# Kernel optimization log

Measured on AMD Instinct MI355X. Metric: run time of the kernel, lower is better.

## Reference

```python
import jax, jax.numpy as jnp
import numpy as np

EPS = 1e-5
K = 3

def _bn(x, g, b):
    # training-mode BatchNorm2d: batch stats over (N,H,W), biased variance
    m = jnp.mean(x, axis=(0, 2, 3), keepdims=True)
    v = jnp.var(x, axis=(0, 2, 3), keepdims=True)
    return (x - m) * jax.lax.rsqrt(v + EPS) * g[None, :, None, None] + b[None, :, None, None]

def _gelu(x):
    return jax.nn.gelu(x, approximate=False)

def _dyn_dw(x, aw1, ab1, aw2, ab2):
    # dynamic depthwise conv: per-sample k^2 softmax weights shared over channels
    b, c, h, w = x.shape
    gap = jnp.mean(x, axis=(2, 3))                              # (b,c)
    h1 = jax.nn.relu(jnp.einsum('oc,bc->bo', aw1, gap) + ab1)   # (b,c//8)
    kw = jax.nn.softmax(jnp.einsum('oc,bc->bo', aw2, h1) + ab2, axis=1)  # (b,k^2)
    xp = jnp.pad(x, ((0, 0), (0, 0), (1, 1), (1, 1)))
    out = jnp.zeros_like(x)
    idx = 0
    for i in range(K):
        for j in range(K):
            out = out + kw[:, idx, None, None, None] * xp[:, :, i:i + h, j:j + w]
            idx += 1
    return out

def _channel_att(x, w1, w2):
    avg = jnp.mean(x, axis=(2, 3))        # (b,C)
    mx = jnp.max(x, axis=(2, 3))          # (b,C)
    def fc(v):
        return jnp.einsum('oc,bc->bo', w2, jax.nn.relu(jnp.einsum('oc,bc->bo', w1, v)))
    s = jax.nn.sigmoid(fc(avg) + fc(mx))  # (b,C)
    return s[:, :, None, None] * x

def _forward(x, w1, b1, g1, be1, aw1, ab1, aw2, ab2, g2, be2,
             ca_w1, ca_w2, pw, pb, g3, be3, sw, sb):
    b, n, d = x.shape
    h = w = int(np.sqrt(n))
    residual = x
    xi = jnp.transpose(x.reshape(b, h, w, d), (0, 3, 1, 2))       # (b,d,h,w)
    # pw_expand: 1x1 conv -> GELU -> BN
    y = jnp.einsum('oc,bchw->bohw', w1, xi) + b1[None, :, None, None]
    y = _bn(_gelu(y), g1, be1)                                    # (b,4d,h,w)
    # dw_conv: dynamic depthwise -> GELU -> BN -> channel attention
    y = _dyn_dw(y, aw1, ab1, aw2, ab2)
    y = _bn(_gelu(y), g2, be2)
    y = _channel_att(y, ca_w1, ca_w2)
    # spatial attention
    avg_o = jnp.mean(y, axis=1, keepdims=True)
    max_o = jnp.max(y, axis=1, keepdims=True)
    sp_in = jnp.concatenate([avg_o, max_o], axis=1)               # (b,2,h,w)
    sp = jax.lax.conv_general_dilated(sp_in, sw, (1, 1), ((3, 3), (3, 3)),
                                      dimension_numbers=('NCHW', 'OIHW', 'NCHW'))
    sp = jax.nn.sigmoid(sp + sb[None, :, None, None])
    y = y * sp
    # pw_project: 1x1 conv -> BN
    y = jnp.einsum('oc,bchw->bohw', pw, y) + pb[None, :, None, None]
    y = _bn(y, g3, be3)
    y = jnp.transpose(y, (0, 2, 3, 1)).reshape(b, n, d)
    return residual + y

def setup_inputs() -> dict:
    key = jax.random.key(0)
    ks = jax.random.split(key, 16)
    d, C = 256, 1024
    def rn(k, shape, fan):
        return jax.random.normal(k, shape, jnp.float32) * np.float32(np.sqrt(2.0 / fan))
    return {
        'x': jax.random.normal(ks[0], (8, 1024, d), jnp.float32),
        'w1': rn(ks[1], (C, d), d), 'b1': jnp.zeros((C,), jnp.float32),
        'g1': jnp.ones((C,), jnp.float32), 'be1': jnp.zeros((C,), jnp.float32),
        'aw1': rn(ks[2], (C // 8, C), C), 'ab1': jnp.zeros((C // 8,), jnp.float32),
        'aw2': rn(ks[3], (K * K, C // 8), C // 8), 'ab2': jnp.zeros((K * K,), jnp.float32),
        'g2': jnp.ones((C,), jnp.float32), 'be2': jnp.zeros((C,), jnp.float32),
        'ca_w1': rn(ks[4], (C // 16, C), C), 'ca_w2': rn(ks[5], (C, C // 16), C // 16),
        'pw': rn(ks[6], (d, C), C), 'pb': jnp.zeros((d,), jnp.float32),
        'g3': jnp.ones((d,), jnp.float32), 'be3': jnp.zeros((d,), jnp.float32),
        'sw': rn(ks[7], (1, 2, 7, 7), 2 * 49), 'sb': jnp.zeros((1,), jnp.float32),
    }

def reference(x, w1, b1, g1, be1, aw1, ab1, aw2, ab2, g2, be2,
              ca_w1, ca_w2, pw, pb, g3, be3, sw, sb):
    return _forward(x, w1, b1, g1, be1, aw1, ab1, aw2, ab2, g2, be2,
                    ca_w1, ca_w2, pw, pb, g3, be3, sw, sb)
```

## Files before the change

### kernel.cpp

```cpp
#include <hip/hip_runtime.h>
#include <math.h>

constexpr int B = 8;
constexpr int D = 256;
constexpr int C = 1024;
constexpr int H = 32, W = 32;
constexpr int P = H * W;
constexpr int M = B * P;
constexpr float EPS = 1e-5f;

typedef unsigned short u16;
typedef unsigned int u32;
typedef __attribute__((ext_vector_type(8))) short short8;
typedef __attribute__((ext_vector_type(4))) float floatx4;

constexpr size_t WS_CHSUM1 = 0;
constexpr size_t WS_CHSQ1  = 1024;
constexpr size_t WS_GAPSUM = 2048;
constexpr size_t WS_CHSUM3 = 10240;
constexpr size_t WS_CHSQ3  = 10496;
constexpr size_t WS_CHSUM2 = 10752;
constexpr size_t WS_CHSQ2  = 11776;
constexpr size_t WS_BSUM2  = 12800;
constexpr size_t WS_UMAX2  = 20992;
constexpr size_t WS_UMAXN2 = 29184;
constexpr size_t WS_ACC_COUNT = 37376;
constexpr size_t WS_SCALE1 = 37376;
constexpr size_t WS_SHIFT1 = 38400;
constexpr size_t WS_KW     = 39424;
constexpr size_t WS_SCALE2 = 39680;
constexpr size_t WS_SHIFT2 = 40704;
constexpr size_t WS_SATT   = 41728;
constexpr size_t WS_AVGO   = 49920;
constexpr size_t WS_MAXO   = 58112;
constexpr size_t WS_SP     = 66304;
constexpr size_t WS_PRE    = 74496;
constexpr size_t WS_T1B    = 2171648;
constexpr size_t WS_T2B    = 6365952;
constexpr size_t WS_XB     = 10560256;
constexpr size_t WS_W1B    = 11608832;
constexpr size_t WS_PWB    = 11739904;
constexpr size_t WS_PWBF   = 11870976;
constexpr size_t WS_BIAS2  = 12919552;

__device__ __forceinline__ float gelu_exact(float v) {
    return 0.5f * v * (1.0f + erff(v * 0.70710678118654752440f));
}

__device__ __forceinline__ u16 f2bf(float f) {
    u32 u = __float_as_uint(f);
    u += 0x7fff + ((u >> 16) & 1);
    return (u16)(u >> 16);
}

__device__ __forceinline__ float bf2f(u16 v) {
    return __uint_as_float(((u32)v) << 16);
}

__device__ __forceinline__ u32 fkey(float f) {
    u32 u = __float_as_uint(f);
    return (u & 0x80000000u) ? ~u : (u | 0x80000000u);
}
__device__ __forceinline__ float fkeyinv(u32 k) {
    return __uint_as_float((k & 0x80000000u) ? (k ^ 0x80000000u) : ~k);
}

#define GLOAD(SRC, DST) __builtin_amdgcn_global_load_lds( \
    (const __attribute__((address_space(1))) void*)(SRC), \
    (__attribute__((address_space(3))) void*)(DST), 16, 0, 0)

__global__ __launch_bounds__(256) void cvt_all_kernel(const float* __restrict__ x,
                                                      const float* __restrict__ w1,
                                                      u16* __restrict__ xb,
                                                      u16* __restrict__ w1b,
                                                      float* __restrict__ acc_zero) {
    const int i = blockIdx.x * 256 + threadIdx.x;
    if (i < (int)WS_ACC_COUNT) acc_zero[i] = 0.f;
    const float* src;
    u16* dst;
    int off;
    if (i < 524288) { src = x;  dst = xb;  off = i; }
    else            { src = w1; dst = w1b; off = i - 524288; }
    const float4 v = *(const float4*)(src + (size_t)off * 4);
    uint2 o;
    o.x = ((u32)f2bf(v.x)) | ((u32)f2bf(v.y) << 16);
    o.y = ((u32)f2bf(v.z)) | ((u32)f2bf(v.w) << 16);
    *(uint2*)(dst + (size_t)off * 4) = o;
}

template<int KD, int EPI, int NS, int MB, int NB>
__global__ __launch_bounds__(256) void mfma_gemm_kernel(
    const u16* __restrict__ A,
    const u16* __restrict__ Bw,
    const float* __restrict__ bias,
    const float* __restrict__ bias_post,
    const float* __restrict__ avg_o,
    const float* __restrict__ max_o,
    const float* __restrict__ swp,
    const float* __restrict__ sbp,
    void* __restrict__ outv,
    float* __restrict__ csum,
    float* __restrict__ csq,
    float* __restrict__ gsum)
{
    constexpr int MI = MB / 32;
    constexpr int NJ = NB / 32;
    constexpr int ABUF = MB * 32;
    constexpr int BBUF = NB * 32;
    constexpr int BUFSZ = ABUF + BBUF;
    constexpr int GA = MB / 64;
    constexpr int GB = NB / 64;
    constexpr int LD = GA + GB;
    static_assert(LD == 3, "vmcnt literals assume 3 loads per chunk");
    constexpr int NCH = KD / 32;
    constexpr int GX = NS / NB;
    constexpr int NWG = (M / MB) * GX;
    constexpr int CPX = NWG / 8;
    extern __shared__ u16 smem[];
    const int t = threadIdx.x;
    const int lane = t & 63;

    const int lin = blockIdx.y * GX + blockIdx.x;
    const int swz = (lin & 7) * CPX + (lin >> 3);
    const int bx = swz % GX;
    const int by = swz / GX;
    const int row0 = by * MB;
    const int col0 = bx * NB;
    const int bb = row0 >> 10;

    const int wv = t >> 6;
    const int wrow = (wv >> 1) * (MB / 2);
    const int wcol = (wv & 1) * (NB / 2);
    const int lm = lane & 15;
    const int lk8 = (lane >> 4) * 8;
    const int srow = t >> 2;
    const int scol = (t & 3) * 8;
    const u16* gA = A + (size_t)(row0 + srow) * KD + scol;
    const u16* gB = Bw + (EPI == 1 ? (size_t)bb * NS * KD : (size_t)0)
                       + (size_t)(col0 + srow) * KD + scol;
    const float* biasp = bias + (EPI == 1 ? bb * NS : 0);

    const floatx4 zero = {0.f, 0.f, 0.f, 0.f};
    floatx4 acc[MI][NJ];
#pragma unroll
    for (int i = 0; i < MI; ++i)
#pragma unroll
        for (int j = 0; j < NJ; ++j) acc[i][j] = zero;

    auto stage = [&](u16* buf, int c) {
        const int kk = c * 32;
        u16* As = buf;
        u16* Bs = buf + ABUF;
#pragma unroll
        for (int g = 0; g < GA; ++g)
            GLOAD(gA + (size_t)g * 64 * KD + kk, As + g * 2048 + t * 8);
#pragma unroll
        for (int g = 0; g < GB; ++g)
            GLOAD(gB + (size_t)g * 64 * KD + kk, Bs + g * 2048 + t * 8);
    };
    auto compute = [&](const u16* buf) {
        const u16* As = buf;
        const u16* Bs = buf + ABUF;
        short8 af[MI], bf[NJ];
#pragma unroll
        for (int i = 0; i < MI; ++i)
            af[i] = *(const short8*)(As + (wrow + i * 16 + lm) * 32 + lk8);
#pragma unroll
        for (int j = 0; j < NJ; ++j)
            bf[j] = *(const short8*)(Bs + (wcol + j * 16 + lm) * 32 + lk8);
#pragma unroll
        for (int i = 0; i < MI; ++i)
#pragma unroll
            for (int j = 0; j < NJ; ++j)
                acc[i][j] = __builtin_amdgcn_mfma_f32_16x16x32_bf16(af[i], bf[j], acc[i][j], 0, 0, 0);
    };

    stage(smem, 0);
    if (NCH > 1) stage(smem + BUFSZ, 1);

    float* ext = (float*)smem + 9216;
    if constexpr (EPI == 1) {
        const int p0 = (by & 7) * MB;
        const int h0 = p0 >> 5;
        const int bbase = bb * P;
        for (int e = t; e < 640; e += 256) {
            const bool isM = e >= 320;
            const int idx = isM ? e - 320 : e;
            const int r = idx >> 5, w = idx & 31;
            const int hh = h0 - 3 + r;
            float v = 0.f;
            if (hh >= 0 && hh < H) v = (isM ? max_o : avg_o)[bbase + hh * W + w];
            ext[e] = v;
        }
        if (t < 98) ext[640 + t] = swp[t];
        __syncthreads();
        if (t < 128) {
            const int hl = t >> 5, w = t & 31;
            float a = sbp[0];
#pragma unroll
            for (int i = 0; i < 7; ++i) {
                const int r = hl + i;
#pragma unroll
                for (int j = 0; j < 7; ++j) {
                    const int ww = w + j - 3;
                    if (ww < 0 || ww >= W) continue;
                    a = fmaf(ext[640 + i * 7 + j], ext[r * 32 + ww], a);
                    a = fmaf(ext[640 + 49 + i * 7 + j], ext[320 + r * 32 + ww], a);
                }
            }
            ext[768 + t] = 1.0f / (1.0f + expf(-a));
        }
    }

    int cur = 0;
    for (int c = 0; c < NCH; ++c) {
        if (c + 2 < NCH) {
            const int nb3 = (cur + 2 >= 3) ? cur - 1 : cur + 2;
            stage(smem + nb3 * BUFSZ, c + 2);
            asm volatile("s_waitcnt vmcnt(6)" ::: "memory");
        } else if (c + 1 < NCH) {
            asm volatile("s_waitcnt vmcnt(3)" ::: "memory");
        } else {
            asm volatile("s_waitcnt vmcnt(0)" ::: "memory");
        }
        __builtin_amdgcn_s_barrier();
        compute(smem + cur * BUFSZ);
        asm volatile("s_waitcnt lgkmcnt(0)" ::: "memory");
        __builtin_amdgcn_s_barrier();
        cur = (cur + 1 >= 3) ? 0 : cur + 1;
    }

    float colsum[NJ], colsq[NJ];
#pragma unroll
    for (int j = 0; j < NJ; ++j) { colsum[j] = 0.f; colsq[j] = 0.f; }

    if (EPI == 0) {
        u16* Cs = smem;
#pragma unroll
        for (int i = 0; i < MI; ++i) {
#pragma unroll
            for (int r = 0; r < 4; ++r) {
                const int lrow = wrow + i * 16 + (lane >> 4) * 4 + r;
#pragma unroll
                for (int j = 0; j < NJ; ++j) {
                    const int lcol = wcol + j * 16 + lm;
                    const float tv = gelu_exact(acc[i][j][r] + biasp[col0 + lcol]);
                    Cs[lrow * NB + lcol] = f2bf(tv);
                    colsum[j] += tv;
                    colsq[j] = fmaf(tv, tv, colsq[j]);
                }
            }
        }
        __syncthreads();
        constexpr int TPR = NB / 8;
        constexpr int RPP = 256 / TPR;
        u16* outp = (u16*)outv;
#pragma unroll
        for (int pp = 0; pp < MB / RPP; ++pp) {
            const int r = pp * RPP + t / TPR;
            const int cc = (t % TPR) * 8;
            *(uint4*)(outp + (size_t)(row0 + r) * NS + col0 + cc) =
                *(const uint4*)(Cs + r * NB + cc);
        }
    } else {
        float* Cs = (float*)smem;
#pragma unroll
        for (int i = 0; i < MI; ++i) {
#pragma unroll
            for (int r = 0; r < 4; ++r) {
                const int lrow = wrow + i * 16 + (lane >> 4) * 4 + r;
                const float rs = ext[768 + lrow];
#pragma unroll
                for (int j = 0; j < NJ; ++j) {
                    const int lcol = wcol + j * 16 + lm;
                    const float tv = rs * (acc[i][j][r] + biasp[col0 + lcol])
                                   + bias_post[col0 + lcol];
                    Cs[lrow * NB + lcol] = tv;
                    colsum[j] += tv;
                    colsq[j] = fmaf(tv, tv, colsq[j]);
                }
            }
        }
        __syncthreads();
        constexpr int TPR = NB / 4;
        constexpr int RPP = 256 / TPR;
        float* outp = (float*)outv;
#pragma unroll
        for (int pp = 0; pp < MB / RPP; ++pp) {
            const int r = pp * RPP + t / TPR;
            const int cc = (t % TPR) * 4;
            *(float4*)(outp + (size_t)(row0 + r) * NS + col0 + cc) =
                *(const float4*)(Cs + r * NB + cc);
        }
    }

#pragma unroll
    for (int j = 0; j < NJ; ++j) {
        float s = colsum[j];
        float q = colsq[j];
        s += __shfl_xor(s, 16); s += __shfl_xor(s, 32);
        q += __shfl_xor(q, 16); q += __shfl_xor(q, 32);
        if (lane < 16) {
            const int c = col0 + wcol + j * 16 + lm;
            atomicAdd(&csum[c], s);
            atomicAdd(&csq[c], q);
            if (EPI == 0) atomicAdd(&gsum[bb * NS + c], s);
        }
    }
}

__global__ __launch_bounds__(1024) void dynmlp_kernel(const float* __restrict__ chsum1,
                                                      const float* __restrict__ chsq1,
                                                      const float* __restrict__ gapsum,
                                                      const float* __restrict__ g1,
                                                      const float* __restrict__ be1,
                                                      const float* __restrict__ aw1,
                                                      const float* __restrict__ ab1,
                                                      const float* __restrict__ aw2,
                                                      const float* __restrict__ ab2,
                                                      float* __restrict__ scale1,
                                                      float* __restrict__ shift1,
                                                      float* __restrict__ kw) {
    const int b = blockIdx.x;
    const int t = threadIdx.x;
    const int wave = t >> 6, lane = t & 63;
    __shared__ float g[1024];
    __shared__ float h1[128];
    __shared__ float logits[12];
    {
        const float m = chsum1[t] * (1.0f / (float)M);
        const float var = chsq1[t] * (1.0f / (float)M) - m * m;
        const float rstd = rsqrtf(var + EPS);
        const float sc = rstd * g1[t];
        const float sh = be1[t] - m * sc;
        if (b == 0) { scale1[t] = sc; shift1[t] = sh; }
        g[t] = gapsum[b * C + t] * (1.0f / (float)P) * sc + sh;
    }
    __syncthreads();
#pragma unroll
    for (int k = 0; k < 8; ++k) {
        const int u = wave * 8 + k;
        const float4* wr = (const float4*)(aw1 + (size_t)u * C);
        float s = 0.f;
#pragma unroll
        for (int ch = 0; ch < 4; ++ch) {
            const float4 wv = wr[lane + 64 * ch];
            const float4 sv = *(const float4*)(g + 4 * lane + 256 * ch);
            s += wv.x * sv.x + wv.y * sv.y + wv.z * sv.z + wv.w * sv.w;
        }
#pragma unroll
        for (int off = 1; off < 64; off <<= 1) s += __shfl_xor(s, off);
        if (lane == 0) h1[u] = fmaxf(s + ab1[u], 0.f);
    }
    __syncthreads();
    if (wave < 9) {
        float s = aw2[wave * 128 + lane] * h1[lane]
                + aw2[wave * 128 + 64 + lane] * h1[64 + lane];
#pragma unroll
        for (int off = 1; off < 64; off <<= 1) s += __shfl_xor(s, off);
        if (lane == 0) logits[wave] = s + ab2[wave];
    }
    __syncthreads();
    if (t == 0) {
        float mx = logits[0];
        for (int i = 1; i < 9; ++i) mx = fmaxf(mx, logits[i]);
        float e[9], den = 0.f;
        for (int i = 0; i < 9; ++i) { e[i] = expf(logits[i] - mx); den += e[i]; }
        const float inv = 1.0f / den;
        for (int i = 0; i < 9; ++i) kw[b * 9 + i] = e[i] * inv;
    }
}

__global__ __launch_bounds__(256) void dwconv_kernel(const u16* __restrict__ t1b,
                                                     const float* __restrict__ scale1,
                                                     const float* __restrict__ shift1,
                                                     const float* __restrict__ kw,
                                                     u16* __restrict__ t2b,
                                                     float* __restrict__ chsum2,
                                                     float* __restrict__ chsq2,
                                                     float* __restrict__ bsum2,
                                                     u32* __restrict__ umax2,
                                                     u32* __restrict__ umaxn2) {
    __shared__ u16 rows[3 * 32 * 256];
    const int lin = blockIdx.y * 4 + blockIdx.x;
    const int xcd = lin & 7;
    const int i7 = lin >> 3;
    const int b = i7 >> 4;
    const int r4 = i7 & 15;
    const int h = xcd * 4 + (r4 >> 2);
    const int cq = r4 & 3;
    const int t = threadIdx.x;

    const u16* gbase = t1b + (size_t)b * P * C + cq * 256;
#pragma unroll
    for (int i = 0; i < 12; ++i) {
        const int lin2 = i * 256 + t;
        const int chunk = lin2 >> 5;
        const int r = chunk >> 5;
        const int w = chunk & 31;
        const int off8 = (lin2 & 31) * 8;
        const int hr = h + r - 1;
        uint4 v = {0u, 0u, 0u, 0u};
        if (hr >= 0 && hr < H)
            v = *(const uint4*)(gbase + (size_t)(hr * W + w) * C + off8);
        *(uint4*)(&rows[chunk * 256 + off8]) = v;
    }
    __syncthreads();

    const int c = t;
    const int gc = cq * 256 + c;
    float kk[9];
#pragma unroll
    for (int i = 0; i < 9; ++i) kk[i] = kw[b * 9 + i];
    const float sc = scale1[gc];
    const float sh = shift1[gc];
    float scm[3], shm[3];
    scm[0] = (h > 0)     ? sc : 0.f;  shm[0] = (h > 0)     ? sh : 0.f;
    scm[1] = sc;                      shm[1] = sh;
    scm[2] = (h < H - 1) ? sc : 0.f;  shm[2] = (h < H - 1) ? sh : 0.f;

    const u16* rp0 = rows + c;
#define DWVAL(ri, w) fmaf(bf2f(rp0[((ri) * 32 + (w)) * 256]), scm[ri], shm[ri])

    float vm0 = 0.f, vm1 = 0.f, vm2 = 0.f;
    float vc0 = DWVAL(0, 0), vc1 = DWVAL(1, 0), vc2 = DWVAL(2, 0);
    float vp0 = DWVAL(0, 1), vp1 = DWVAL(1, 1), vp2 = DWVAL(2, 1);

    float s = 0.f, q = 0.f, mx = -INFINITY, mn = INFINITY;
    u16* orow = t2b + ((size_t)b * P + h * W) * C + gc;
    for (int w = 0; w < W; ++w) {
        float acc;
        acc = kk[0] * vm0;
        acc = fmaf(kk[1], vc0, acc);
        acc = fmaf(kk[2], vp0, acc);
        acc = fmaf(kk[3], vm1, acc);
        acc = fmaf(kk[4], vc1, acc);
        acc = fmaf(kk[5], vp1, acc);
        acc = fmaf(kk[6], vm2, acc);
        acc = fmaf(kk[7], vc2, acc);
        acc = fmaf(kk[8], vp2, acc);
        const float y = gelu_exact(acc);
        orow[(size_t)w * C] = f2bf(y);
        s += y;
        q = fmaf(y, y, q);
        mx = fmaxf(mx, y);
        mn = fminf(mn, y);
        vm0 = vc0; vc0 = vp0;
        vm1 = vc1; vc1 = vp1;
        vm2 = vc2; vc2 = vp2;
        if (w + 2 < W) {
            vp0 = DWVAL(0, w + 2);
            vp1 = DWVAL(1, w + 2);
            vp2 = DWVAL(2, w + 2);
        } else {
            vp0 = 0.f; vp1 = 0.f; vp2 = 0.f;
        }
    }
#undef DWVAL
    atomicAdd(&chsum2[gc], s);
    atomicAdd(&chsq2[gc], q);
    atomicAdd(&bsum2[b * C + gc], s);
    atomicMax(&umax2[b * C + gc], fkey(mx));
    atomicMax(&umaxn2[b * C + gc], fkey(-mn));
}

__global__ __launch_bounds__(1024) void chatt_kernel(const float* __restrict__ chsum2,
                                                     const float* __restrict__ chsq2,
                                                     const float* __restrict__ bsum2,
                                                     const u32* __restrict__ umax2,
                                                     const u32* __restrict__ umaxn2,
                                                     const float* __restrict__ g2,
                                                     const float* __restrict__ be2,
                                                     const float* __restrict__ caw1,
                                                     const float* __restrict__ caw2,
                                                     float* __restrict__ scale2,
                                                     float* __restrict__ shift2,
                                                     float* __restrict__ s_att) {
    const int b = blockIdx.x;
    const int t = threadIdx.x;
    const int wave = t >> 6, lane = t & 63;
    __shared__ float la[1024], lx[1024], ha[64], hm[64];
    {
        const float m = chsum2[t] * (1.0f / (float)M);
        const float var = chsq2[t] * (1.0f / (float)M) - m * m;
        const float rstd = rsqrtf(var + EPS);
        const float sc = rstd * g2[t];
        const float sh = be2[t] - m * sc;
        if (b == 0) { scale2[t] = sc; shift2[t] = sh; }
        la[t] = bsum2[b * C + t] * (1.0f / (float)P) * sc + sh;
        const float mx = fkeyinv(umax2[b * C + t]);
        const float mn = -fkeyinv(umaxn2[b * C + t]);
        lx[t] = (sc >= 0.f ? mx : mn) * sc + sh;
    }
    __syncthreads();
#pragma unroll
    for (int k = 0; k < 8; ++k) {
        const int u = wave * 8 + k;
        const int row = u & 63;
        const float* src = (u < 64) ? la : lx;
        const float4* wr = (const float4*)(caw1 + (size_t)row * C);
        float s = 0.f;
#pragma unroll
        for (int ch = 0; ch < 4; ++ch) {
            const float4 wv = wr[lane + 64 * ch];
            const float4 sv = *(const float4*)(src + 4 * lane + 256 * ch);
            s += wv.x * sv.x + wv.y * sv.y + wv.z * sv.z + wv.w * sv.w;
        }
#pragma unroll
        for (int off = 1; off < 64; off <<= 1) s += __shfl_xor(s, off);
        if (lane == 0) {
            s = fmaxf(s, 0.f);
            if (u < 64) ha[row] = s; else hm[row] = s;
        }
    }
    __syncthreads();
    {
        const float4* w2 = (const float4*)(caw2 + (size_t)t * 64);
        float s = 0.f;
#pragma unroll
        for (int j = 0; j < 16; ++j) {
            const float4 wv = w2[j];
            s += wv.x * (ha[j * 4 + 0] + hm[j * 4 + 0]);
            s += wv.y * (ha[j * 4 + 1] + hm[j * 4 + 1]);
            s += wv.z * (ha[j * 4 + 2] + hm[j * 4 + 2]);
            s += wv.w * (ha[j * 4 + 3] + hm[j * 4 + 3]);
        }
        s_att[b * C + t] = 1.0f / (1.0f + expf(-s));
    }
}

__global__ __launch_bounds__(256) void yqfold_kernel(const u16* __restrict__ t2b,
                                                     const float* __restrict__ scale2,
                                                     const float* __restrict__ shift2,
                                                     const float* __restrict__ s_att,
                                                     const float* __restrict__ pw,
                                                     float* __restrict__ avg_o,
                                                     float* __restrict__ max_o,
                                                     u16* __restrict__ pwb,
                                                     float* __restrict__ bias2) {
    const int bid = blockIdx.x;
    const int t = threadIdx.x;
    const int wave = t >> 6, lane = t & 63;
    __shared__ float r0[4], r1[4];
    if (bid < M) {
        const int row = bid;
        const int b = row >> 10;
        const int c0 = t * 4;
        const uint2 vv = *(const uint2*)(t2b + (size_t)row * C + c0);
        const float v0 = bf2f((u16)(vv.x & 0xffff));
        const float v1 = bf2f((u16)(vv.x >> 16));
        const float v2 = bf2f((u16)(vv.y & 0xffff));
        const float v3 = bf2f((u16)(vv.y >> 16));
        const float4 sc = *(const float4*)(scale2 + c0);
        const float4 sh = *(const float4*)(shift2 + c0);
        const float4 sa = *(const float4*)(s_att + (size_t)b * C + c0);
        const float y0 = fmaf(v0, sc.x, sh.x) * sa.x;
        const float y1 = fmaf(v1, sc.y, sh.y) * sa.y;
        const float y2 = fmaf(v2, sc.z, sh.z) * sa.z;
        const float y3 = fmaf(v3, sc.w, sh.w) * sa.w;
        float s = (y0 + y1) + (y2 + y3);
        float mx = fmaxf(fmaxf(y0, y1), fmaxf(y2, y3));
#pragma unroll
        for (int off = 32; off > 0; off >>= 1) {
            s += __shfl_down(s, off);
            mx = fmaxf(mx, __shfl_down(mx, off));
        }
        if (lane == 0) { r0[wave] = s; r1[wave] = mx; }
        __syncthreads();
        if (t == 0) {
            const float S = r0[0] + r0[1] + r0[2] + r0[3];
            const float Mx = fmaxf(fmaxf(r1[0], r1[1]), fmaxf(r1[2], r1[3]));
            avg_o[row] = S * (1.0f / (float)C);
            max_o[row] = Mx;
        }
    } else {
        const int bd = bid - M;
        const int b = bd >> 8;
        const int d = bd & 255;
        const int c0 = t * 4;
        const float4 wv = *(const float4*)(pw + (size_t)d * C + c0);
        const float4 sc = *(const float4*)(scale2 + c0);
        const float4 sh = *(const float4*)(shift2 + c0);
        const float4 sa = *(const float4*)(s_att + (size_t)b * C + c0);
        uint2 o;
        o.x = ((u32)f2bf(wv.x * sc.x * sa.x)) | ((u32)f2bf(wv.y * sc.y * sa.y) << 16);
        o.y = ((u32)f2bf(wv.z * sc.z * sa.z)) | ((u32)f2bf(wv.w * sc.w * sa.w) << 16);
        *(uint2*)(pwb + ((size_t)b * D + d) * C + c0) = o;
        float s = wv.x * sh.x * sa.x + wv.y * sh.y * sa.y
                + wv.z * sh.z * sa.z + wv.w * sh.w * sa.w;
#pragma unroll
        for (int off = 1; off < 64; off <<= 1) s += __shfl_xor(s, off);
        if (lane == 0) r0[wave] = s;
        __syncthreads();
        if (t == 0) bias2[bd] = r0[0] + r0[1] + r0[2] + r0[3];
    }
}

__global__ __launch_bounds__(256) void final_kernel(const float* __restrict__ x,
                                                    const float* __restrict__ pre,
                                                    const float* __restrict__ chsum3,
                                                    const float* __restrict__ chsq3,
                                                    const float* __restrict__ g3,
                                                    const float* __restrict__ be3,
                                                    float* __restrict__ out) {
    __shared__ float lsc[256], lsh[256];
    const int t = threadIdx.x;
    {
        const float m = chsum3[t] * (1.0f / (float)M);
        const float var = chsq3[t] * (1.0f / (float)M) - m * m;
        const float rstd = rsqrtf(var + EPS);
        const float sc = rstd * g3[t];
        lsc[t] = sc;
        lsh[t] = be3[t] - m * sc;
    }
    __syncthreads();
    const int i = blockIdx.x * 256 + t;
    const int e = i * 4;
    const int d = e & 255;
    const float4 xv = *(const float4*)(x + e);
    const float4 pv = *(const float4*)(pre + e);
    const float4 sc = *(const float4*)(lsc + d);
    const float4 sh = *(const float4*)(lsh + d);
    float4 o;
    o.x = xv.x + fmaf(pv.x, sc.x, sh.x);
    o.y = xv.y + fmaf(pv.y, sc.y, sh.y);
    o.z = xv.z + fmaf(pv.z, sc.z, sh.z);
    o.w = xv.w + fmaf(pv.w, sc.w, sh.w);
    *(float4*)(out + e) = o;
}

extern "C" void kernel_launch(void* const* d_in, const int* in_sizes, int n_in,
                              void* d_out, int out_size, void* d_ws, size_t ws_size,
                              hipStream_t stream) {
    const float* x    = (const float*)d_in[0];
    const float* w1   = (const float*)d_in[1];
    const float* b1   = (const float*)d_in[2];
    const float* g1   = (const float*)d_in[3];
    const float* be1  = (const float*)d_in[4];
    const float* aw1  = (const float*)d_in[5];
    const float* ab1  = (const float*)d_in[6];
    const float* aw2  = (const float*)d_in[7];
    const float* ab2  = (const float*)d_in[8];
    const float* g2   = (const float*)d_in[9];
    const float* be2  = (const float*)d_in[10];
    const float* caw1 = (const float*)d_in[11];
    const float* caw2 = (const float*)d_in[12];
    const float* pw   = (const float*)d_in[13];
    const float* pb   = (const float*)d_in[14];
    const float* g3   = (const float*)d_in[15];
    const float* be3  = (const float*)d_in[16];
    const float* sw   = (const float*)d_in[17];
    const float* sb   = (const float*)d_in[18];
    float* out = (float*)d_out;
    float* ws = (float*)d_ws;

    float* chsum1  = ws + WS_CHSUM1;
    float* chsq1   = ws + WS_CHSQ1;
    float* gapsum  = ws + WS_GAPSUM;
    float* chsum3  = ws + WS_CHSUM3;
    float* chsq3   = ws + WS_CHSQ3;
    float* chsum2  = ws + WS_CHSUM2;
    float* chsq2   = ws + WS_CHSQ2;
    float* bsum2   = ws + WS_BSUM2;
    u32*   umax2   = (u32*)(ws + WS_UMAX2);
    u32*   umaxn2  = (u32*)(ws + WS_UMAXN2);
    float* scale1  = ws + WS_SCALE1;
    float* shift1  = ws + WS_SHIFT1;
    float* kw      = ws + WS_KW;
    float* scale2  = ws + WS_SCALE2;
    float* shift2  = ws + WS_SHIFT2;
    float* s_att   = ws + WS_SATT;
    float* avg_o   = ws + WS_AVGO;
    float* max_o   = ws + WS_MAXO;
    float* pre     = ws + WS_PRE;
    float* bias2   = ws + WS_BIAS2;
    u16* t1b  = (u16*)(ws + WS_T1B);
    u16* t2b  = (u16*)(ws + WS_T2B);
    u16* xb   = (u16*)(ws + WS_XB);
    u16* w1b  = (u16*)(ws + WS_W1B);
    u16* pwbf = (u16*)(ws + WS_PWBF);

    cvt_all_kernel<<<dim3(2304), 256, 0, stream>>>(x, w1, xb, w1b, ws);
    mfma_gemm_kernel<256, 0, C, 128, 64><<<dim3(C / 64, M / 128), 256, 36864, stream>>>(
        xb, w1b, b1, nullptr, nullptr, nullptr, nullptr, nullptr,
        t1b, chsum1, chsq1, gapsum);
    dynmlp_kernel<<<dim3(B), 1024, 0, stream>>>(chsum1, chsq1, gapsum, g1, be1,
                                                aw1, ab1, aw2, ab2, scale1, shift1, kw);
    dwconv_kernel<<<dim3(4, B * H), 256, 0, stream>>>(t1b, scale1, shift1, kw, t2b,
                                                      chsum2, chsq2, bsum2, umax2, umaxn2);
    chatt_kernel<<<dim3(B), 1024, 0, stream>>>(chsum2, chsq2, bsum2, umax2, umaxn2,
                                               g2, be2, caw1, caw2, scale2, shift2, s_att);
    yqfold_kernel<<<dim3(M + B * D), 256, 0, stream>>>(t2b, scale2, shift2, s_att, pw,
                                                       avg_o, max_o, pwbf, bias2);
    mfma_gemm_kernel<1024, 1, D, 128, 64><<<dim3(D / 64, M / 128), 256, 40448, stream>>>(
        t2b, pwbf, bias2, pb, avg_o, max_o, sw, sb,
        pre, chsum3, chsq3, nullptr);
    final_kernel<<<dim3((M * D / 4) / 256), 256, 0, stream>>>(x, pre, chsum3, chsq3, g3, be3, out);
}
```

Measured before the change: 198.9 us.

## Split K across two wave groups in the second GEMM with LDS reduction

Adds a WSPLIT template parameter so the projection GEMM (K=1024, only 256 workgroups) runs with 512 threads. Two independent 4-wave groups each pipeline half of the K chunks in their own LDS buffers, then partial accumulators are summed through shared memory before the epilogue. This aims to raise occupancy and latency hiding for a GEMM with few tiles. In exchange it uses roughly double the LDS per block and adds an extra reduction pass with barriers.

```diff
diff --git a/kernel.cpp b/kernel.cpp
--- a/kernel.cpp
+++ b/kernel.cpp
@@ -88,8 +88,8 @@
     *(uint2*)(dst + (size_t)off * 4) = o;
 }
 
-template<int KD, int EPI, int NS, int MB, int NB>
-__global__ __launch_bounds__(256) void mfma_gemm_kernel(
+template<int KD, int EPI, int NS, int MB, int NB, int WSPLIT>
+__global__ __launch_bounds__(256 * WSPLIT) void mfma_gemm_kernel(
     const u16* __restrict__ A,
     const u16* __restrict__ Bw,
     const float* __restrict__ bias,
@@ -103,6 +103,7 @@
     float* __restrict__ csq,
     float* __restrict__ gsum)
 {
+    constexpr int NT = 256 * WSPLIT;
     constexpr int MI = MB / 32;
     constexpr int NJ = NB / 32;
     constexpr int ABUF = MB * 32;
@@ -113,12 +114,17 @@
     constexpr int LD = GA + GB;
     static_assert(LD == 3, "vmcnt literals assume 3 loads per chunk");
     constexpr int NCH = KD / 32;
+    constexpr int NCHG = NCH / WSPLIT;
     constexpr int GX = NS / NB;
     constexpr int NWG = (M / MB) * GX;
     constexpr int CPX = NWG / 8;
     extern __shared__ u16 smem[];
     const int t = threadIdx.x;
     const int lane = t & 63;
+    const int wv = t >> 6;
+    const int grp = (WSPLIT == 2) ? (wv >> 2) : 0;
+    const int wg = wv & 3;
+    const int tg = t & 255;
 
     const int lin = blockIdx.y * GX + blockIdx.x;
     const int swz = (lin & 7) * CPX + (lin >> 3);
@@ -128,18 +134,20 @@
     const int col0 = bx * NB;
     const int bb = row0 >> 10;
 
-    const int wv = t >> 6;
-    const int wrow = (wv >> 1) * (MB / 2);
-    const int wcol = (wv & 1) * (NB / 2);
+    const int wrow = (wg >> 1) * (MB / 2);
+    const int wcol = (wg & 1) * (NB / 2);
     const int lm = lane & 15;
     const int lk8 = (lane >> 4) * 8;
-    const int srow = t >> 2;
-    const int scol = (t & 3) * 8;
+    const int srow = tg >> 2;
+    const int scol = (tg & 3) * 8;
     const u16* gA = A + (size_t)(row0 + srow) * KD + scol;
     const u16* gB = Bw + (EPI == 1 ? (size_t)bb * NS * KD : (size_t)0)
                        + (size_t)(col0 + srow) * KD + scol;
     const float* biasp = bias + (EPI == 1 ? bb * NS : 0);
 
+    u16* gsmem = smem + grp * (3 * BUFSZ);
+    const int kbase = grp * NCHG;
+
     const floatx4 zero = {0.f, 0.f, 0.f, 0.f};
     floatx4 acc[MI][NJ];
 #pragma unroll
@@ -148,15 +156,15 @@
         for (int j = 0; j < NJ; ++j) acc[i][j] = zero;
 
     auto stage = [&](u16* buf, int c) {
-        const int kk = c * 32;
+        const int kk = (kbase + c) * 32;
         u16* As = buf;
         u16* Bs = buf + ABUF;
 #pragma unroll
         for (int g = 0; g < GA; ++g)
-            GLOAD(gA + (size_t)g * 64 * KD + kk, As + g * 2048 + t * 8);
+            GLOAD(gA + (size_t)g * 64 * KD + kk, As + g * 2048 + tg * 8);
 #pragma unroll
         for (int g = 0; g < GB; ++g)
-            GLOAD(gB + (size_t)g * 64 * KD + kk, Bs + g * 2048 + t * 8);
+            GLOAD(gB + (size_t)g * 64 * KD + kk, Bs + g * 2048 + tg * 8);
     };
     auto compute = [&](const u16* buf) {
         const u16* As = buf;
@@ -175,15 +183,15 @@
                 acc[i][j] = __builtin_amdgcn_mfma_f32_16x16x32_bf16(af[i], bf[j], acc[i][j], 0, 0, 0);
     };
 
-    stage(smem, 0);
-    if (NCH > 1) stage(smem + BUFSZ, 1);
-
-    float* ext = (float*)smem + 9216;
+    stage(gsmem, 0);
+    if (NCHG > 1) stage(gsmem + BUFSZ, 1);
+
+    float* ext = (float*)(smem + (size_t)WSPLIT * 3 * BUFSZ);
     if constexpr (EPI == 1) {
         const int p0 = (by & 7) * MB;
         const int h0 = p0 >> 5;
         const int bbase = bb * P;
-        for (int e = t; e < 640; e += 256) {
+        for (int e = t; e < 640; e += NT) {
             const bool isM = e >= 320;
             const int idx = isM ? e - 320 : e;
             const int r = idx >> 5, w = idx & 31;
@@ -213,21 +221,49 @@
     }
 
     int cur = 0;
-    for (int c = 0; c < NCH; ++c) {
-        if (c + 2 < NCH) {
+    for (int c = 0; c < NCHG; ++c) {
+        if (c + 2 < NCHG) {
             const int nb3 = (cur + 2 >= 3) ? cur - 1 : cur + 2;
-            stage(smem + nb3 * BUFSZ, c + 2);
+            stage(gsmem + nb3 * BUFSZ, c + 2);
             asm volatile("s_waitcnt vmcnt(6)" ::: "memory");
-        } else if (c + 1 < NCH) {
+        } else if (c + 1 < NCHG) {
             asm volatile("s_waitcnt vmcnt(3)" ::: "memory");
         } else {
             asm volatile("s_waitcnt vmcnt(0)" ::: "memory");
         }
         __builtin_amdgcn_s_barrier();
-        compute(smem + cur * BUFSZ);
+        compute(gsmem + cur * BUFSZ);
         asm volatile("s_waitcnt lgkmcnt(0)" ::: "memory");
         __builtin_amdgcn_s_barrier();
         cur = (cur + 1 >= 3) ? 0 : cur + 1;
+    }
+
+    if constexpr (WSPLIT == 2) {
+        float* red = (float*)(smem + 3 * BUFSZ);
+        if (grp == 1) {
+#pragma unroll
+            for (int i = 0; i < MI; ++i)
+#pragma unroll
+                for (int r = 0; r < 4; ++r) {
+                    const int lrow = wrow + i * 16 + (lane >> 4) * 4 + r;
+#pragma unroll
+                    for (int j = 0; j < NJ; ++j)
+                        red[lrow * NB + wcol + j * 16 + lm] = acc[i][j][r];
+                }
+        }
+        __syncthreads();
+        if (grp == 0) {
+#pragma unroll
+            for (int i = 0; i < MI; ++i)
+#pragma unroll
+                for (int r = 0; r < 4; ++r) {
+                    const int lrow = wrow + i * 16 + (lane >> 4) * 4 + r;
+#pragma unroll
+                    for (int j = 0; j < NJ; ++j)
+                        acc[i][j][r] += red[lrow * NB + wcol + j * 16 + lm];
+                }
+        }
+        __syncthreads();
     }
 
     float colsum[NJ], colsq[NJ];
@@ -253,7 +289,7 @@
         }
         __syncthreads();
         constexpr int TPR = NB / 8;
-        constexpr int RPP = 256 / TPR;
+        constexpr int RPP = NT / TPR;
         u16* outp = (u16*)outv;
 #pragma unroll
         for (int pp = 0; pp < MB / RPP; ++pp) {
@@ -264,26 +300,28 @@
         }
     } else {
         float* Cs = (float*)smem;
-#pragma unroll
-        for (int i = 0; i < MI; ++i) {
-#pragma unroll
-            for (int r = 0; r < 4; ++r) {
-                const int lrow = wrow + i * 16 + (lane >> 4) * 4 + r;
-                const float rs = ext[768 + lrow];
-#pragma unroll
-                for (int j = 0; j < NJ; ++j) {
-                    const int lcol = wcol + j * 16 + lm;
-                    const float tv = rs * (acc[i][j][r] + biasp[col0 + lcol])
-                                   + bias_post[col0 + lcol];
-                    Cs[lrow * NB + lcol] = tv;
-                    colsum[j] += tv;
-                    colsq[j] = fmaf(tv, tv, colsq[j]);
+        if (grp == 0) {
+#pragma unroll
+            for (int i = 0; i < MI; ++i) {
+#pragma unroll
+                for (int r = 0; r < 4; ++r) {
+                    const int lrow = wrow + i * 16 + (lane >> 4) * 4 + r;
+                    const float rs = ext[768 + lrow];
+#pragma unroll
+                    for (int j = 0; j < NJ; ++j) {
+                        const int lcol = wcol + j * 16 + lm;
+                        const float tv = rs * (acc[i][j][r] + biasp[col0 + lcol])
+                                       + bias_post[col0 + lcol];
+                        Cs[lrow * NB + lcol] = tv;
+                        colsum[j] += tv;
+                        colsq[j] = fmaf(tv, tv, colsq[j]);
+                    }
                 }
             }
         }
         __syncthreads();
         constexpr int TPR = NB / 4;
-        constexpr int RPP = 256 / TPR;
+        constexpr int RPP = NT / TPR;
         float* outp = (float*)outv;
 #pragma unroll
         for (int pp = 0; pp < MB / RPP; ++pp) {
@@ -300,7 +338,7 @@
         float q = colsq[j];
         s += __shfl_xor(s, 16); s += __shfl_xor(s, 32);
         q += __shfl_xor(q, 16); q += __shfl_xor(q, 32);
-        if (lane < 16) {
+        if (grp == 0 && lane < 16) {
             const int c = col0 + wcol + j * 16 + lm;
             atomicAdd(&csum[c], s);
             atomicAdd(&csq[c], q);
@@ -681,7 +719,7 @@
     u16* pwbf = (u16*)(ws + WS_PWBF);
 
     cvt_all_kernel<<<dim3(2304), 256, 0, stream>>>(x, w1, xb, w1b, ws);
-    mfma_gemm_kernel<256, 0, C, 128, 64><<<dim3(C / 64, M / 128), 256, 36864, stream>>>(
+    mfma_gemm_kernel<256, 0, C, 128, 64, 1><<<dim3(C / 64, M / 128), 256, 36864, stream>>>(
         xb, w1b, b1, nullptr, nullptr, nullptr, nullptr, nullptr,
         t1b, chsum1, chsq1, gapsum);
     dynmlp_kernel<<<dim3(B), 1024, 0, stream>>>(chsum1, chsq1, gapsum, g1, be1,
@@ -692,7 +730,7 @@
                                                g2, be2, caw1, caw2, scale2, shift2, s_att);
     yqfold_kernel<<<dim3(M + B * D), 256, 0, stream>>>(t2b, scale2, shift2, s_att, pw,
                                                        avg_o, max_o, pwbf, bias2);
-    mfma_gemm_kernel<1024, 1, D, 128, 64><<<dim3(D / 64, M / 128), 256, 40448, stream>>>(
+    mfma_gemm_kernel<1024, 1, D, 128, 64, 2><<<dim3(D / 64, M / 128), 512, 77312, stream>>>(
         t2b, pwbf, bias2, pb, avg_o, max_o, sw, sb,
         pre, chsum3, chsq3, nullptr);
     final_kernel<<<dim3((M * D / 4) / 256), 256, 0, stream>>>(x, pre, chsum3, chsq3, g3, be3, out);
```

Result: no change. 197.6 us (-0.6%).
